# Optimization experiments

Hardware: AMD Instinct MI355X
Metric: run time of the kernel (lower is better)

Reference implementation:

```python
import jax, jax.numpy as jnp
import numpy as np

B, S, D_IN, D_H = 4, 4096, 512, 64

def setup_inputs() -> dict:
    key = jax.random.key(0)
    ks = jax.random.split(key, 7)
    std = 1.0 / np.sqrt(D_IN)
    x = jax.random.normal(ks[0], (B, S, D_IN), dtype=jnp.float32)
    Wq = jax.random.uniform(ks[1], (D_IN, D_H), jnp.float32, -std, std)
    bq = jax.random.uniform(ks[2], (D_H,), jnp.float32, -std, std)
    Wk = jax.random.uniform(ks[3], (D_IN, D_H), jnp.float32, -std, std)
    bk = jax.random.uniform(ks[4], (D_H,), jnp.float32, -std, std)
    Wv = jax.random.uniform(ks[5], (D_IN, D_H), jnp.float32, -std, std)
    bv = jax.random.uniform(ks[6], (D_H,), jnp.float32, -std, std)
    return {"x": x, "Wq": Wq, "bq": bq, "Wk": Wk, "bk": bk, "Wv": Wv, "bv": bv}

def reference(x, Wq, bq, Wk, bk, Wv, bv):
    # q,k,v: [B, S, D_H]
    q = jnp.einsum('bsi,ih->bsh', x, Wq) + bq
    k = jnp.einsum('bsi,ih->bsh', x, Wk) + bk
    v = jnp.einsum('bsi,ih->bsh', x, Wv) + bv
    scale = 1.0 / jnp.sqrt(jnp.asarray(D_H, dtype=q.dtype))
    scores = jnp.einsum('bqh,bkh->bqk', q, k) * scale  # [B, S, S]
    att = jax.nn.softmax(scores, axis=-1)
    return jnp.einsum('bqk,bkh->bqh', att, v)
```

## Files before the change

### kernel.cpp

```cpp
#include <hip/hip_runtime.h>
#include <hip/hip_bf16.h>
#include <stdint.h>

#define LOG2E 1.4426950408889634f
#define SEQ 4096
#define DIN 512
#define DH 64
#define NSPLIT 8
#define QSCALE (0.125f * LOG2E)

typedef __attribute__((ext_vector_type(8))) short short8;
typedef __attribute__((ext_vector_type(16))) float f32x16;
typedef __attribute__((ext_vector_type(4))) float f32x4;

static __device__ __forceinline__ uint16_t f2bf(float f){
  uint32_t u = __float_as_uint(f);
  uint32_t r = u + 0x7fffu + ((u >> 16) & 1u);
  return (uint16_t)(r >> 16);
}

static __device__ __forceinline__ uint32_t cvt_pk_bf16(float lo, float hi){
  uint32_t d;
  asm("v_cvt_pk_bf16_f32 %0, %1, %2" : "=v"(d) : "v"(lo), "v"(hi));
  return d;
}

static __device__ __forceinline__ void perm32swap(uint32_t &a, uint32_t &b){
  asm("v_permlane32_swap_b32 %0, %1" : "+v"(a), "+v"(b));
}

static __device__ __forceinline__ float xadd32(float v){ return v + __shfl_xor(v, 32); }

static __device__ __forceinline__ void gload_lds16(const void* g, void* l){
  __builtin_amdgcn_global_load_lds(
      (const __attribute__((address_space(1))) unsigned int*)g,
      (__attribute__((address_space(3))) unsigned int*)l, 16, 0, 0);
}

__global__ void packw_kernel(const float* __restrict__ Wq, const float* __restrict__ Wk,
                             const float* __restrict__ Wv, uint4* __restrict__ Wp){
  int t0 = blockIdx.x * 256 + threadIdx.x;
  int lane = t0 & 63;
  int grp = t0 >> 6;
  int w3 = grp >> 6;
  int t  = (grp >> 2) & 15;
  int nc = grp & 3;
  const float* W = (w3 == 0) ? Wq : ((w3 == 1) ? Wk : Wv);
  int g = lane >> 4, cc = lane & 15;
  int k0 = t * 32 + g * 8;
  int n  = nc * 16 + cc;
  uint32_t o[4];
  #pragma unroll
  for (int p = 0; p < 4; ++p){
    float lo = W[(size_t)(k0 + 2*p    ) * DH + n];
    float hi = W[(size_t)(k0 + 2*p + 1) * DH + n];
    o[p] = cvt_pk_bf16(lo, hi);
  }
  Wp[(size_t)grp * 64 + lane] = make_uint4(o[0], o[1], o[2], o[3]);
}

__global__ __launch_bounds__(256) void proj_kernel(
    const float* __restrict__ x, const uint4* __restrict__ Wp,
    const float* __restrict__ bq, const float* __restrict__ bk, const float* __restrict__ bv,
    uint16_t* __restrict__ Qs, uint16_t* __restrict__ Kb, uint16_t* __restrict__ Vt)
{
  __shared__ uint16_t xl[32][520];
  int tid = threadIdx.x, lane = tid & 63, wv = tid >> 6;
  int c = lane & 15, g = lane >> 4;
  int rowbase = blockIdx.x * 32;

  {
    int row = tid >> 3, cb = (tid & 7) * 64;
    const float* src = x + (size_t)(rowbase + row) * DIN + cb;
    #pragma unroll
    for (int i = 0; i < 4; ++i){
      float4 f0 = *(const float4*)(src + i * 16 + 0);
      float4 f1 = *(const float4*)(src + i * 16 + 4);
      float4 f2 = *(const float4*)(src + i * 16 + 8);
      float4 f3 = *(const float4*)(src + i * 16 + 12);
      uint4 w0 = make_uint4(cvt_pk_bf16(f0.x, f0.y), cvt_pk_bf16(f0.z, f0.w),
                            cvt_pk_bf16(f1.x, f1.y), cvt_pk_bf16(f1.z, f1.w));
      uint4 w1 = make_uint4(cvt_pk_bf16(f2.x, f2.y), cvt_pk_bf16(f2.z, f2.w),
                            cvt_pk_bf16(f3.x, f3.y), cvt_pk_bf16(f3.z, f3.w));
      *(uint4*)(&xl[row][cb + i * 16]) = w0;
      *(uint4*)(&xl[row][cb + i * 16 + 8]) = w1;
    }
  }
  __syncthreads();

  f32x4 acc[2][3];
  #pragma unroll
  for (int mt = 0; mt < 2; ++mt)
    #pragma unroll
    for (int j = 0; j < 3; ++j)
      #pragma unroll
      for (int r = 0; r < 4; ++r) acc[mt][j][r] = 0.f;

  #pragma unroll 2
  for (int t = 0; t < 16; ++t){
    short8 xa[2];
    #pragma unroll
    for (int mt = 0; mt < 2; ++mt)
      xa[mt] = *(const short8*)(&xl[mt * 16 + c][t * 32 + g * 8]);
    #pragma unroll
    for (int j = 0; j < 3; ++j){
      int i = wv * 3 + j;
      union { uint4 u; short8 s; } wf;
      wf.u = Wp[(size_t)((i >> 2) * 64 + t * 4 + (i & 3)) * 64 + lane];
      #pragma unroll
      for (int mt = 0; mt < 2; ++mt)
        acc[mt][j] = __builtin_amdgcn_mfma_f32_16x16x32_bf16(xa[mt], wf.s, acc[mt][j], 0, 0, 0);
    }
  }

  #pragma unroll
  for (int mt = 0; mt < 2; ++mt){
    int mb0 = rowbase + mt * 16 + 4 * g;
    #pragma unroll
    for (int j = 0; j < 3; ++j){
      int i = wv * 3 + j;
      int w3 = i >> 2, nc = i & 3, n = nc * 16 + c;
      const float* B = (w3 == 0) ? bq : ((w3 == 1) ? bk : bv);
      float bias = B[n];
      float v0 = acc[mt][j][0] + bias;
      float v1 = acc[mt][j][1] + bias;
      float v2 = acc[mt][j][2] + bias;
      float v3 = acc[mt][j][3] + bias;
      if (w3 == 0){
        Qs[(size_t)(mb0 + 0) * DH + n] = f2bf(v0 * QSCALE);
        Qs[(size_t)(mb0 + 1) * DH + n] = f2bf(v1 * QSCALE);
        Qs[(size_t)(mb0 + 2) * DH + n] = f2bf(v2 * QSCALE);
        Qs[(size_t)(mb0 + 3) * DH + n] = f2bf(v3 * QSCALE);
      } else if (w3 == 1){
        Kb[(size_t)(mb0 + 0) * DH + n] = f2bf(v0);
        Kb[(size_t)(mb0 + 1) * DH + n] = f2bf(v1);
        Kb[(size_t)(mb0 + 2) * DH + n] = f2bf(v2);
        Kb[(size_t)(mb0 + 3) * DH + n] = f2bf(v3);
      } else {
        int b = mb0 >> 12, mloc = mb0 & 4095;
        uint32_t lo = cvt_pk_bf16(v0, v1);
        uint32_t hi = cvt_pk_bf16(v2, v3);
        *(uint2*)(&Vt[((size_t)(b * DH + n)) * SEQ + mloc]) = make_uint2(lo, hi);
      }
    }
  }
}

__global__ __launch_bounds__(256, 3) void attn_kernel(
    const uint16_t* __restrict__ Qs, const uint16_t* __restrict__ Kb,
    const uint16_t* __restrict__ Vt, uint16_t* __restrict__ Pacc,
    float* __restrict__ Pl)
{
  __shared__ uint8_t lds[32768];
  const int tid = threadIdx.x, lane = tid & 63, wv = tid >> 6;
  const int bid = blockIdx.x;
  const int split = bid & 7, batch = (bid >> 3) & 3, qtile = bid >> 5;
  const int c = lane & 31, hi = lane >> 5;
  const int NT = SEQ / NSPLIT / 64;

  const int qrow = batch * SEQ + qtile * 128 + wv * 32 + c;

  short8 qf[4];
  {
    const uint16_t* qp = Qs + (size_t)qrow * DH;
    #pragma unroll
    for (int ks = 0; ks < 4; ++ks){
      union { uint4 u; short8 s; } v;
      v.u = *(const uint4*)(qp + ks * 16 + hi * 8);
      qf[ks] = v.s;
    }
  }

  int addr8[2][4];
  #pragma unroll
  for (int a = 0; a < 2; ++a)
    #pragma unroll
    for (int b = 0; b < 4; ++b)
      addr8[a][b] = (32 * a + c) * 128 + (((2 * b + hi) ^ (c & 7)) << 4);

  const int slotA = wv * 128 + lane, slotB = slotA + 64;
  const int keyA = slotA >> 3, keyB = slotB >> 3;
  const int dgA = (slotA & 7) ^ (keyA & 7), dgB = (slotB & 7) ^ (keyB & 7);
  const uint8_t* Kg = (const uint8_t*)Kb + ((size_t)(batch * SEQ + split * 512)) * (DH * 2);
  const uint8_t* KgA = Kg + keyA * 128 + dgA * 16;
  const uint8_t* KgB = Kg + keyB * 128 + dgB * 16;
  const uint8_t* Vg = (const uint8_t*)Vt + (size_t)batch * (DH * SEQ * 2) + split * 1024;
  const uint8_t* VgA = Vg + keyA * (SEQ * 2) + dgA * 16;
  const uint8_t* VgB = Vg + keyB * (SEQ * 2) + dgB * 16;

  f32x16 acc[2];
  #pragma unroll
  for (int d = 0; d < 2; ++d)
    #pragma unroll
    for (int r = 0; r < 16; ++r) acc[d][r] = 0.f;

  f32x16 ZERO;
  #pragma unroll
  for (int r = 0; r < 16; ++r) ZERO[r] = 0.f;
  asm volatile("" : "+v"(ZERO));

  float l0_ = 0.f, l1_ = 0.f, l2_ = 0.f, l3_ = 0.f;

  gload_lds16(KgA, lds + wv * 2048);
  gload_lds16(KgB, lds + wv * 2048 + 1024);
  gload_lds16(VgA, lds + 8192 + wv * 2048);
  gload_lds16(VgB, lds + 8192 + wv * 2048 + 1024);
  __syncthreads();

  #pragma unroll 1
  for (int t = 0; t < NT; ++t){
    const int OFF = (t & 1) << 14;
    const int NOFF = OFF ^ 16384;

    if (t < NT - 1){
      gload_lds16(KgA + (size_t)(t + 1) * 8192, lds + NOFF + wv * 2048);
      gload_lds16(KgB + (size_t)(t + 1) * 8192, lds + NOFF + wv * 2048 + 1024);
      gload_lds16(VgA + (size_t)(t + 1) * 128,  lds + NOFF + 8192 + wv * 2048);
      gload_lds16(VgB + (size_t)(t + 1) * 128,  lds + NOFF + 8192 + wv * 2048 + 1024);
    }

    f32x16 sa[2];
    __builtin_amdgcn_s_setprio(1);
    #pragma unroll
    for (int st = 0; st < 2; ++st){
      #pragma unroll
      for (int ks = 0; ks < 4; ++ks){
        short8 kf = *(const short8*)(lds + OFF + addr8[st][ks]);
        sa[st] = __builtin_amdgcn_mfma_f32_32x32x16_bf16(
            kf, qf[ks], (ks == 0) ? ZERO : sa[st], 0, 0, 0);
      }
    }
    __builtin_amdgcn_s_setprio(0);

    uint32_t pk[2][8];
    #pragma unroll
    for (int st = 0; st < 2; ++st){
      float pv[16];
      #pragma unroll
      for (int r = 0; r < 16; ++r) pv[r] = __builtin_amdgcn_exp2f(sa[st][r]);
      #pragma unroll
      for (int r = 0; r < 4; ++r){
        l0_ += pv[4 * r + 0];
        l1_ += pv[4 * r + 1];
        l2_ += pv[4 * r + 2];
        l3_ += pv[4 * r + 3];
      }
      #pragma unroll
      for (int p = 0; p < 8; ++p) pk[st][p] = cvt_pk_bf16(pv[2 * p], pv[2 * p + 1]);
    }

    short8 pf[4];
    #pragma unroll
    for (int kslab = 0; kslab < 4; ++kslab){
      int st = kslab >> 1, q4 = (kslab & 1) * 4;
      uint32_t w_[4];
      #pragma unroll
      for (int w1 = 0; w1 < 2; ++w1){
        uint32_t a = pk[st][q4 + w1];
        uint32_t b = pk[st][q4 + 2 + w1];
        perm32swap(a, b);
        w_[w1] = a; w_[2 + w1] = b;
      }
      union { uint32_t u[4]; short8 s; } u_;
      u_.u[0] = w_[0]; u_.u[1] = w_[1]; u_.u[2] = w_[2]; u_.u[3] = w_[3];
      pf[kslab] = u_.s;
    }

    __builtin_amdgcn_s_setprio(1);
    #pragma unroll
    for (int kslab = 0; kslab < 4; ++kslab){
      #pragma unroll
      for (int dst = 0; dst < 2; ++dst){
        short8 vf = *(const short8*)(lds + OFF + 8192 + addr8[dst][kslab]);
        acc[dst] = __builtin_amdgcn_mfma_f32_32x32x16_bf16(vf, pf[kslab], acc[dst], 0, 0, 0);
      }
    }
    __builtin_amdgcn_s_setprio(0);

    __syncthreads();
  }

  uint16_t* pa = Pacc + ((size_t)split * 16384 + qrow) * DH;
  #pragma unroll
  for (int dst = 0; dst < 2; ++dst)
    #pragma unroll
    for (int rq = 0; rq < 4; ++rq){
      uint32_t lo = cvt_pk_bf16(acc[dst][rq * 4 + 0], acc[dst][rq * 4 + 1]);
      uint32_t hi2 = cvt_pk_bf16(acc[dst][rq * 4 + 2], acc[dst][rq * 4 + 3]);
      *(uint2*)(pa + dst * 32 + rq * 8 + hi * 4) = make_uint2(lo, hi2);
    }
  float l_tot = xadd32((l0_ + l1_) + (l2_ + l3_));
  if (hi == 0) Pl[(size_t)split * 16384 + qrow] = l_tot;
}

__global__ __launch_bounds__(256) void combine_kernel(
    const uint16_t* __restrict__ Pacc, const float* __restrict__ Pl,
    float* __restrict__ out)
{
  int t = blockIdx.x * 256 + threadIdx.x;
  int q = t >> 3, part = t & 7;
  float l = 0.f;
  #pragma unroll
  for (int s = 0; s < NSPLIT; ++s) l += Pl[(size_t)s * 16384 + q];
  float inv = 1.0f / l;

  float o[8];
  #pragma unroll
  for (int i = 0; i < 8; ++i) o[i] = 0.f;
  #pragma unroll
  for (int s = 0; s < NSPLIT; ++s){
    const uint16_t* p = Pacc + ((size_t)s * 16384 + q) * DH + part * 8;
    uint4 v = *(const uint4*)(p);
    const uint32_t* w = (const uint32_t*)&v;
    #pragma unroll
    for (int k = 0; k < 4; ++k){
      o[2 * k + 0] += __uint_as_float((w[k] & 0xffffu) << 16);
      o[2 * k + 1] += __uint_as_float((w[k] >> 16) << 16);
    }
  }
  float* ob = out + (size_t)q * DH + part * 8;
  #pragma unroll
  for (int i = 0; i < 2; ++i){
    float4 v = make_float4(o[4*i] * inv, o[4*i+1] * inv, o[4*i+2] * inv, o[4*i+3] * inv);
    *(float4*)(ob + 4 * i) = v;
  }
}

extern "C" void kernel_launch(void* const* d_in, const int* in_sizes, int n_in,
                              void* d_out, int out_size, void* d_ws, size_t ws_size,
                              hipStream_t stream)
{
  (void)in_sizes; (void)n_in; (void)out_size; (void)ws_size;
  const float* x  = (const float*)d_in[0];
  const float* Wq = (const float*)d_in[1];
  const float* bq = (const float*)d_in[2];
  const float* Wk = (const float*)d_in[3];
  const float* bk = (const float*)d_in[4];
  const float* Wv = (const float*)d_in[5];
  const float* bv = (const float*)d_in[6];
  float* out = (float*)d_out;
  uint8_t* ws = (uint8_t*)d_ws;

  const size_t o_Wp = 0;
  const size_t o_Q  = 196608;
  const size_t o_K  = o_Q + 2097152;
  const size_t o_Vt = o_K + 2097152;
  const size_t o_Pa = o_Vt + 2097152;
  const size_t o_Pl = o_Pa + 16777216;

  packw_kernel<<<48, 256, 0, stream>>>(Wq, Wk, Wv, (uint4*)(ws + o_Wp));
  proj_kernel<<<512, 256, 0, stream>>>(x, (const uint4*)(ws + o_Wp), bq, bk, bv,
      (uint16_t*)(ws + o_Q), (uint16_t*)(ws + o_K), (uint16_t*)(ws + o_Vt));
  attn_kernel<<<1024, 256, 0, stream>>>((const uint16_t*)(ws + o_Q), (const uint16_t*)(ws + o_K),
      (const uint16_t*)(ws + o_Vt), (uint16_t*)(ws + o_Pa), (float*)(ws + o_Pl));
  combine_kernel<<<512, 256, 0, stream>>>((const uint16_t*)(ws + o_Pa), (const float*)(ws + o_Pl), out);
}
```

Baseline: 53.72 us.

## Double KV splits and preload each block's whole K/V slice into LDS

Raises the KV split count from 8 to 16, so each attention block handles 256 keys and the grid doubles to 2048 blocks. Each block now loads its entire K and transposed-V slice into 64KB of LDS up front. This replaces the double-buffered per-tile prefetch and removes the per-iteration barriers. It targets better parallelism and sync overhead, but lowers occupancy to 2 blocks, exposes the load latency before any compute, and doubles the partial-result traffic the combine kernel must read.

```diff
diff --git a/kernel.cpp b/kernel.cpp
--- a/kernel.cpp
+++ b/kernel.cpp
@@ -6,7 +6,7 @@
 #define SEQ 4096
 #define DIN 512
 #define DH 64
-#define NSPLIT 8
+#define NSPLIT 16
 #define QSCALE (0.125f * LOG2E)
 
 typedef __attribute__((ext_vector_type(8))) short short8;
@@ -146,15 +146,15 @@
   }
 }
 
-__global__ __launch_bounds__(256, 3) void attn_kernel(
+__global__ __launch_bounds__(256, 2) void attn_kernel(
     const uint16_t* __restrict__ Qs, const uint16_t* __restrict__ Kb,
     const uint16_t* __restrict__ Vt, uint16_t* __restrict__ Pacc,
     float* __restrict__ Pl)
 {
-  __shared__ uint8_t lds[32768];
+  __shared__ uint8_t lds[65536];
   const int tid = threadIdx.x, lane = tid & 63, wv = tid >> 6;
   const int bid = blockIdx.x;
-  const int split = bid & 7, batch = (bid >> 3) & 3, qtile = bid >> 5;
+  const int split = bid & 15, batch = (bid >> 4) & 3, qtile = bid >> 6;
   const int c = lane & 31, hi = lane >> 5;
   const int NT = SEQ / NSPLIT / 64;
 
@@ -178,15 +178,24 @@
     for (int b = 0; b < 4; ++b)
       addr8[a][b] = (32 * a + c) * 128 + (((2 * b + hi) ^ (c & 7)) << 4);
 
-  const int slotA = wv * 128 + lane, slotB = slotA + 64;
-  const int keyA = slotA >> 3, keyB = slotB >> 3;
-  const int dgA = (slotA & 7) ^ (keyA & 7), dgB = (slotB & 7) ^ (keyB & 7);
-  const uint8_t* Kg = (const uint8_t*)Kb + ((size_t)(batch * SEQ + split * 512)) * (DH * 2);
-  const uint8_t* KgA = Kg + keyA * 128 + dgA * 16;
-  const uint8_t* KgB = Kg + keyB * 128 + dgB * 16;
-  const uint8_t* Vg = (const uint8_t*)Vt + (size_t)batch * (DH * SEQ * 2) + split * 1024;
-  const uint8_t* VgA = Vg + keyA * (SEQ * 2) + dgA * 16;
-  const uint8_t* VgB = Vg + keyB * (SEQ * 2) + dgB * 16;
+  const uint8_t* Kg = (const uint8_t*)Kb + ((size_t)(batch * SEQ + split * 256)) * (DH * 2);
+  const uint8_t* Vg = (const uint8_t*)Vt + (size_t)batch * (DH * SEQ * 2) + split * 512;
+
+  #pragma unroll
+  for (int pass = 0; pass < 8; ++pass){
+    int s = pass * 256 + tid;
+    int key = s >> 3, dg = (s & 7) ^ (key & 7);
+    gload_lds16(Kg + key * 128 + dg * 16, lds + pass * 4096 + wv * 1024);
+  }
+  #pragma unroll
+  for (int pass = 0; pass < 8; ++pass){
+    int s = pass * 256 + tid;
+    int t4 = s >> 9, r = (s >> 3) & 63, j = s & 7;
+    gload_lds16(Vg + (size_t)r * (SEQ * 2) + t4 * 128 + ((j ^ (r & 7)) << 4),
+                lds + 32768 + pass * 4096 + wv * 1024);
+  }
+  asm volatile("s_waitcnt vmcnt(0)" ::: "memory");
+  __syncthreads();
 
   f32x16 acc[2];
   #pragma unroll
@@ -201,23 +210,9 @@
 
   float l0_ = 0.f, l1_ = 0.f, l2_ = 0.f, l3_ = 0.f;
 
-  gload_lds16(KgA, lds + wv * 2048);
-  gload_lds16(KgB, lds + wv * 2048 + 1024);
-  gload_lds16(VgA, lds + 8192 + wv * 2048);
-  gload_lds16(VgB, lds + 8192 + wv * 2048 + 1024);
-  __syncthreads();
-
   #pragma unroll 1
   for (int t = 0; t < NT; ++t){
-    const int OFF = (t & 1) << 14;
-    const int NOFF = OFF ^ 16384;
-
-    if (t < NT - 1){
-      gload_lds16(KgA + (size_t)(t + 1) * 8192, lds + NOFF + wv * 2048);
-      gload_lds16(KgB + (size_t)(t + 1) * 8192, lds + NOFF + wv * 2048 + 1024);
-      gload_lds16(VgA + (size_t)(t + 1) * 128,  lds + NOFF + 8192 + wv * 2048);
-      gload_lds16(VgB + (size_t)(t + 1) * 128,  lds + NOFF + 8192 + wv * 2048 + 1024);
-    }
+    const int OFF = t << 13;
 
     f32x16 sa[2];
     __builtin_amdgcn_s_setprio(1);
@@ -271,13 +266,11 @@
     for (int kslab = 0; kslab < 4; ++kslab){
       #pragma unroll
       for (int dst = 0; dst < 2; ++dst){
-        short8 vf = *(const short8*)(lds + OFF + 8192 + addr8[dst][kslab]);
+        short8 vf = *(const short8*)(lds + 32768 + OFF + addr8[dst][kslab]);
         acc[dst] = __builtin_amdgcn_mfma_f32_32x32x16_bf16(vf, pf[kslab], acc[dst], 0, 0, 0);
       }
     }
     __builtin_amdgcn_s_setprio(0);
-
-    __syncthreads();
   }
 
   uint16_t* pa = Pacc + ((size_t)split * 16384 + qrow) * DH;
@@ -346,12 +339,12 @@
   const size_t o_K  = o_Q + 2097152;
   const size_t o_Vt = o_K + 2097152;
   const size_t o_Pa = o_Vt + 2097152;
-  const size_t o_Pl = o_Pa + 16777216;
+  const size_t o_Pl = o_Pa + 33554432;
 
   packw_kernel<<<48, 256, 0, stream>>>(Wq, Wk, Wv, (uint4*)(ws + o_Wp));
   proj_kernel<<<512, 256, 0, stream>>>(x, (const uint4*)(ws + o_Wp), bq, bk, bv,
       (uint16_t*)(ws + o_Q), (uint16_t*)(ws + o_K), (uint16_t*)(ws + o_Vt));
-  attn_kernel<<<1024, 256, 0, stream>>>((const uint16_t*)(ws + o_Q), (const uint16_t*)(ws + o_K),
+  attn_kernel<<<2048, 256, 0, stream>>>((const uint16_t*)(ws + o_Q), (const uint16_t*)(ws + o_K),
       (const uint16_t*)(ws + o_Vt), (uint16_t*)(ws + o_Pa), (float*)(ws + o_Pl));
   combine_kernel<<<512, 256, 0, stream>>>((const uint16_t*)(ws + o_Pa), (const float*)(ws + o_Pl), out);
 }
```

Result: slower. 59.77 us (+11.3%).
